# Kernel optimization log

Measured on AMD Instinct MI355X. Metric: run time of the kernel, lower is better.

The kernel has to match this reference:

```python
import jax, jax.numpy as jnp
import numpy as np

SIGMA = 1.0
TEMPERATURE = 1.0
GAMMA = 1.0 / (2.0 * SIGMA ** 2)


def setup_inputs() -> dict:
    key = jax.random.key(0)
    k1, k2 = jax.random.split(key)
    B, N, D = 8, 1024, 128
    features_nc = jax.random.normal(k1, (B, N, D), dtype=jnp.float32)
    features_c = jax.random.normal(k2, (B, N, D), dtype=jnp.float32)
    return {"features_nc": features_nc, "features_c": features_c}


def reference(features_nc, features_c):
    D = features_nc.shape[-1]
    x = features_nc.reshape(-1, D)   # (K, D)
    y = features_c.reshape(-1, D)    # (K, D)
    K = x.shape[0]
    x_sq = jnp.sum(x * x, axis=1, keepdims=True)          # (K, 1)
    y_sq = jnp.sum(y * y, axis=1, keepdims=True)          # (K, 1)
    sq_dist = x_sq + y_sq.T - 2.0 * jnp.matmul(x, y.T)    # (K, K)
    logits = (-GAMMA / TEMPERATURE) * sq_dist
    # cross-entropy with labels = arange(K): mean over rows of -log_softmax diag
    log_probs = jax.nn.log_softmax(logits, axis=-1)
    diag = jnp.diagonal(log_probs)
    loss = -jnp.mean(diag)
    return loss
```

## Files before the change

kernel.cpp:

```cpp
#include <hip/hip_runtime.h>
#include <hip/hip_bf16.h>
#include <math.h>

#define KROWS 8192
#define DDIM  128
#define RT    128
#define CTILE 128
#define NTILES 64
#define NRB   64
#define NC0   12
#define TILEB (CTILE * DDIM * 2)
#define SHIFT 94.0f

static constexpr float LOG2E_F = 1.44269504088896340736f;
static constexpr float LN2_F   = 0.69314718055994530942f;

typedef __attribute__((ext_vector_type(8))) short short8;
typedef __attribute__((ext_vector_type(4))) float float4v;

#if __has_builtin(__builtin_amdgcn_exp2f)
#define EXP2(x) __builtin_amdgcn_exp2f(x)
#else
#define EXP2(x) exp2f(x)
#endif

#define AS1C(p) ((const __attribute__((address_space(1))) void*)(p))
#define AS3(p)  ((__attribute__((address_space(3))) void*)(p))

static __device__ __forceinline__ unsigned short f2bf(float f) {
    __hip_bfloat16 h = __float2bfloat16(f);
    return *reinterpret_cast<unsigned short*>(&h);
}

__global__ __launch_bounds__(256) void prep_kernel(
    const float* __restrict__ x, const float* __restrict__ y,
    unsigned int* __restrict__ xb, unsigned int* __restrict__ yb,
    float* __restrict__ xsq2, float* __restrict__ ysq2,
    float* __restrict__ diagn, float* __restrict__ pl)
{
    const int w = threadIdx.x >> 6, lane = threadIdx.x & 63;
    const int row = blockIdx.x * 4 + w;
    if (blockIdx.x < KROWS / 256) pl[blockIdx.x * 256 + threadIdx.x] = 0.0f;
    const float2 xv = *reinterpret_cast<const float2*>(x + (size_t)row * DDIM + lane * 2);
    const float2 yv = *reinterpret_cast<const float2*>(y + (size_t)row * DDIM + lane * 2);
    xb[(size_t)row * 64 + lane] = (unsigned int)f2bf(xv.x * LOG2E_F)
                                | ((unsigned int)f2bf(xv.y * LOG2E_F) << 16);
    yb[(size_t)row * 64 + lane] = (unsigned int)f2bf(yv.x) | ((unsigned int)f2bf(yv.y) << 16);
    float xx = xv.x * xv.x + xv.y * xv.y;
    float yy = yv.x * yv.x + yv.y * yv.y;
    float xy = xv.x * yv.x + xv.y * yv.y;
    #pragma unroll
    for (int o = 32; o > 0; o >>= 1) {
        xx += __shfl_xor(xx, o, 64);
        yy += __shfl_xor(yy, o, 64);
        xy += __shfl_xor(xy, o, 64);
    }
    if (lane == 0) {
        xsq2[row] = fmaf(-0.5f * xx, LOG2E_F, SHIFT);
        ysq2[row] = -0.5f * yy * LOG2E_F;
        diagn[row] = xy - 0.5f * (xx + yy);
    }
}

__global__ __launch_bounds__(256, 2) void gemm_lse_kernel(
    const unsigned short* __restrict__ xb, const unsigned short* __restrict__ yb,
    const float* __restrict__ xsq2, const float* __restrict__ ysq2,
    float* __restrict__ pl)
{
    __shared__ alignas(16) unsigned char Ys[TILEB];

    const int t = threadIdx.x;
    const int w = t >> 6, lane = t & 63, quad = lane >> 4, lo = lane & 15;
    const int rb = (blockIdx.x & (NRB - 1)) * RT;
    const int c0 = blockIdx.x >> 6;

    short8 af[2][4];
    #pragma unroll
    for (int ri = 0; ri < 2; ri++)
        #pragma unroll
        for (int kk = 0; kk < 4; kk++)
            af[ri][kk] = *reinterpret_cast<const short8*>(
                xb + (size_t)(rb + w * 32 + ri * 16 + lo) * DDIM + kk * 32 + quad * 8);

    float a2v[8];
    #pragma unroll
    for (int ri = 0; ri < 2; ri++)
        #pragma unroll
        for (int r = 0; r < 4; r++)
            a2v[ri * 4 + r] = xsq2[rb + w * 32 + ri * 16 + quad * 4 + r];

    float sums[8];
    #pragma unroll
    for (int i = 0; i < 8; i++) sums[i] = 0.0f;

    const int gswz = ((t >> 4) << 8) + (((t & 15) ^ ((t >> 4) & 7)) << 4);
    int base_k[4];
    #pragma unroll
    for (int kk = 0; kk < 4; kk++)
        base_k[kk] = lo * 256 + ((((kk << 2) + quad) ^ (lo & 7)) << 4);

    {
        const char* g = (const char*)yb + (size_t)c0 * TILEB + gswz;
        #pragma unroll
        for (int q = 0; q < 8; q++)
            __builtin_amdgcn_global_load_lds(AS1C(g + q * 4096),
                                             AS3(&Ys[(q * 256 + t) * 16]), 16, 0, 0);
    }
    __syncthreads();

    int ct = c0;
    while (true) {
        float b2[8];
        #pragma unroll
        for (int ci = 0; ci < 8; ci++) b2[ci] = ysq2[ct * CTILE + ci * 16 + lo];

        float4v acc[2][8];
        #pragma unroll
        for (int ri = 0; ri < 2; ri++)
            #pragma unroll
            for (int ci = 0; ci < 8; ci++)
                acc[ri][ci] = (float4v){a2v[ri * 4 + 0] + b2[ci], a2v[ri * 4 + 1] + b2[ci],
                                        a2v[ri * 4 + 2] + b2[ci], a2v[ri * 4 + 3] + b2[ci]};

        #pragma unroll
        for (int kk = 0; kk < 4; kk++) {
            #pragma unroll
            for (int ci = 0; ci < 8; ci++) {
                short8 b = *reinterpret_cast<const short8*>(&Ys[base_k[kk] + ci * 4096]);
                acc[0][ci] = __builtin_amdgcn_mfma_f32_16x16x32_bf16(af[0][kk], b, acc[0][ci], 0, 0, 0);
                acc[1][ci] = __builtin_amdgcn_mfma_f32_16x16x32_bf16(af[1][kk], b, acc[1][ci], 0, 0, 0);
            }
        }
        __syncthreads();

        const int ctn = ct + NC0;
        if (ctn < NTILES) {
            const char* g = (const char*)yb + (size_t)ctn * TILEB + gswz;
            #pragma unroll
            for (int q = 0; q < 8; q++)
                __builtin_amdgcn_global_load_lds(AS1C(g + q * 4096),
                                                 AS3(&Ys[(q * 256 + t) * 16]), 16, 0, 0);
        }

        #pragma unroll
        for (int ri = 0; ri < 2; ri++)
            #pragma unroll
            for (int r = 0; r < 4; r++) {
                float s = 0.0f;
                #pragma unroll
                for (int ci = 0; ci < 8; ci++)
                    s += EXP2(acc[ri][ci][r]);
                sums[ri * 4 + r] += s;
            }

        if (ctn >= NTILES) break;
        ct = ctn;
        __syncthreads();
    }

    #pragma unroll
    for (int i = 0; i < 8; i++) {
        float s = sums[i];
        s += __shfl_xor(s, 1, 64);
        s += __shfl_xor(s, 2, 64);
        s += __shfl_xor(s, 4, 64);
        s += __shfl_xor(s, 8, 64);
        if (lo == 0) {
            int row = rb + w * 32 + (i >> 2) * 16 + quad * 4 + (i & 3);
            atomicAdd(&pl[row], s);
        }
    }
}

__global__ __launch_bounds__(1024) void finish_kernel(
    const float* __restrict__ pl, const float* __restrict__ diagn,
    float* __restrict__ out)
{
    const int t = threadIdx.x;
    float acc = 0.0f;
    for (int r = t; r < KROWS; r += 1024)
        acc += (log2f(pl[r]) - SHIFT) * LN2_F - diagn[r];
    #pragma unroll
    for (int o = 32; o > 0; o >>= 1) acc += __shfl_down(acc, o, 64);
    __shared__ float ws[16];
    if ((t & 63) == 0) ws[t >> 6] = acc;
    __syncthreads();
    if (t == 0) {
        float s = 0.0f;
        #pragma unroll
        for (int i = 0; i < 16; i++) s += ws[i];
        out[0] = s * (1.0f / KROWS);
    }
}

extern "C" void kernel_launch(void* const* d_in, const int* in_sizes, int n_in,
                              void* d_out, int out_size, void* d_ws, size_t ws_size,
                              hipStream_t stream) {
    const float* x = (const float*)d_in[0];
    const float* y = (const float*)d_in[1];
    float* out = (float*)d_out;

    unsigned short* xb = (unsigned short*)d_ws;
    unsigned short* yb = xb + (size_t)KROWS * DDIM;
    float* xsq2  = (float*)(yb + (size_t)KROWS * DDIM);
    float* ysq2  = xsq2 + KROWS;
    float* diagn = ysq2 + KROWS;
    float* pl    = diagn + KROWS;

    prep_kernel<<<KROWS / 4, 256, 0, stream>>>(x, y, (unsigned int*)xb, (unsigned int*)yb,
                                               xsq2, ysq2, diagn, pl);
    gemm_lse_kernel<<<NRB * NC0, 256, 0, stream>>>(xb, yb, xsq2, ysq2, pl);
    finish_kernel<<<1, 1024, 0, stream>>>(pl, diagn, out);
}
```

Before: 87.56 us.

## Double-buffer Y tiles in LDS and interleave exp with MFMA per column chunk

Replaces the single LDS Y tile with two buffers so the next tile's global-to-LDS load is issued before computing on the current one, dropping one barrier per iteration. It reduces column-split blocks from 12 to 8, so each block processes exactly 8 tiles in a fully unrolled loop. It also restructures the inner loop to finish each 16-column chunk's MFMAs and exponentials before moving on, shrinking the accumulator set and letting exp work overlap matrix ops. The cost is double the LDS footprint, which may limit occupancy, and fewer total blocks (512 vs 768), which may leave CUs underused.

```diff
diff --git a/kernel.cpp b/kernel.cpp
--- a/kernel.cpp
+++ b/kernel.cpp
@@ -8,7 +8,7 @@
 #define CTILE 128
 #define NTILES 64
 #define NRB   64
-#define NC0   12
+#define NC0   8
 #define TILEB (CTILE * DDIM * 2)
 #define SHIFT 94.0f
 
@@ -67,13 +67,24 @@
     const float* __restrict__ xsq2, const float* __restrict__ ysq2,
     float* __restrict__ pl)
 {
-    __shared__ alignas(16) unsigned char Ys[TILEB];
+    __shared__ alignas(16) unsigned char Ys0[TILEB];
+    __shared__ alignas(16) unsigned char Ys1[TILEB];
 
     const int t = threadIdx.x;
     const int w = t >> 6, lane = t & 63, quad = lane >> 4, lo = lane & 15;
     const int rb = (blockIdx.x & (NRB - 1)) * RT;
     const int c0 = blockIdx.x >> 6;
 
+    const int gswz = ((t >> 4) << 8) + (((t & 15) ^ ((t >> 4) & 7)) << 4);
+
+    {
+        const char* g = (const char*)yb + (size_t)c0 * TILEB + gswz;
+        #pragma unroll
+        for (int q = 0; q < 8; q++)
+            __builtin_amdgcn_global_load_lds(AS1C(g + q * 4096),
+                                             AS3(&Ys0[(q * 256 + t) * 16]), 16, 0, 0);
+    }
+
     short8 af[2][4];
     #pragma unroll
     for (int ri = 0; ri < 2; ri++)
@@ -89,73 +100,69 @@
         for (int r = 0; r < 4; r++)
             a2v[ri * 4 + r] = xsq2[rb + w * 32 + ri * 16 + quad * 4 + r];
 
-    float sums[8];
-    #pragma unroll
-    for (int i = 0; i < 8; i++) sums[i] = 0.0f;
-
-    const int gswz = ((t >> 4) << 8) + (((t & 15) ^ ((t >> 4) & 7)) << 4);
+    float b2[8];
+    #pragma unroll
+    for (int ci = 0; ci < 8; ci++) b2[ci] = ysq2[c0 * CTILE + ci * 16 + lo];
+
     int base_k[4];
     #pragma unroll
     for (int kk = 0; kk < 4; kk++)
         base_k[kk] = lo * 256 + ((((kk << 2) + quad) ^ (lo & 7)) << 4);
 
-    {
-        const char* g = (const char*)yb + (size_t)c0 * TILEB + gswz;
-        #pragma unroll
-        for (int q = 0; q < 8; q++)
-            __builtin_amdgcn_global_load_lds(AS1C(g + q * 4096),
-                                             AS3(&Ys[(q * 256 + t) * 16]), 16, 0, 0);
-    }
+    float sums[8];
+    #pragma unroll
+    for (int i = 0; i < 8; i++) sums[i] = 0.0f;
+
     __syncthreads();
 
-    int ct = c0;
-    while (true) {
-        float b2[8];
-        #pragma unroll
-        for (int ci = 0; ci < 8; ci++) b2[ci] = ysq2[ct * CTILE + ci * 16 + lo];
-
-        float4v acc[2][8];
-        #pragma unroll
-        for (int ri = 0; ri < 2; ri++)
-            #pragma unroll
-            for (int ci = 0; ci < 8; ci++)
-                acc[ri][ci] = (float4v){a2v[ri * 4 + 0] + b2[ci], a2v[ri * 4 + 1] + b2[ci],
-                                        a2v[ri * 4 + 2] + b2[ci], a2v[ri * 4 + 3] + b2[ci]};
-
-        #pragma unroll
-        for (int kk = 0; kk < 4; kk++) {
-            #pragma unroll
-            for (int ci = 0; ci < 8; ci++) {
-                short8 b = *reinterpret_cast<const short8*>(&Ys[base_k[kk] + ci * 4096]);
-                acc[0][ci] = __builtin_amdgcn_mfma_f32_16x16x32_bf16(af[0][kk], b, acc[0][ci], 0, 0, 0);
-                acc[1][ci] = __builtin_amdgcn_mfma_f32_16x16x32_bf16(af[1][kk], b, acc[1][ci], 0, 0, 0);
-            }
-        }
-        __syncthreads();
-
-        const int ctn = ct + NC0;
-        if (ctn < NTILES) {
+    #pragma unroll
+    for (int k = 0; k < 8; k++) {
+        const unsigned char* cur = (k & 1) ? Ys1 : Ys0;
+        unsigned char*       nxt = (k & 1) ? Ys0 : Ys1;
+
+        float b2n[8];
+        if (k < 7) {
+            const int ctn = c0 + (k + 1) * NC0;
+            #pragma unroll
+            for (int ci = 0; ci < 8; ci++) b2n[ci] = ysq2[ctn * CTILE + ci * 16 + lo];
             const char* g = (const char*)yb + (size_t)ctn * TILEB + gswz;
             #pragma unroll
             for (int q = 0; q < 8; q++)
                 __builtin_amdgcn_global_load_lds(AS1C(g + q * 4096),
-                                                 AS3(&Ys[(q * 256 + t) * 16]), 16, 0, 0);
-        }
-
-        #pragma unroll
-        for (int ri = 0; ri < 2; ri++)
+                                                 AS3(&nxt[(q * 256 + t) * 16]), 16, 0, 0);
+        }
+
+        float tsum[8];
+        #pragma unroll
+        for (int i = 0; i < 8; i++) tsum[i] = 0.0f;
+
+        #pragma unroll
+        for (int ci = 0; ci < 8; ci++) {
+            float4v a0 = (float4v){a2v[0] + b2[ci], a2v[1] + b2[ci],
+                                   a2v[2] + b2[ci], a2v[3] + b2[ci]};
+            float4v a1 = (float4v){a2v[4] + b2[ci], a2v[5] + b2[ci],
+                                   a2v[6] + b2[ci], a2v[7] + b2[ci]};
+            #pragma unroll
+            for (int kk = 0; kk < 4; kk++) {
+                short8 b = *reinterpret_cast<const short8*>(&cur[base_k[kk] + ci * 4096]);
+                a0 = __builtin_amdgcn_mfma_f32_16x16x32_bf16(af[0][kk], b, a0, 0, 0, 0);
+                a1 = __builtin_amdgcn_mfma_f32_16x16x32_bf16(af[1][kk], b, a1, 0, 0, 0);
+            }
             #pragma unroll
             for (int r = 0; r < 4; r++) {
-                float s = 0.0f;
-                #pragma unroll
-                for (int ci = 0; ci < 8; ci++)
-                    s += EXP2(acc[ri][ci][r]);
-                sums[ri * 4 + r] += s;
+                tsum[r]     += EXP2(a0[r]);
+                tsum[4 + r] += EXP2(a1[r]);
             }
-
-        if (ctn >= NTILES) break;
-        ct = ctn;
-        __syncthreads();
+        }
+
+        #pragma unroll
+        for (int i = 0; i < 8; i++) sums[i] += tsum[i];
+
+        if (k < 7) {
+            #pragma unroll
+            for (int ci = 0; ci < 8; ci++) b2[ci] = b2n[ci];
+            __syncthreads();
+        }
     }
 
     #pragma unroll
```

Result: slower. 167.8 us (+91.6%).

## Restructure tile loop per column group to cut registers and raise occupancy

Applied to the files above, without the earlier changes.

Reorders the inner GEMM loop so each 16-column group runs its full k-reduction and is exponentiated right away, rather than keeping all 16 accumulators live across the tile. This shrinks accumulator register pressure enough to request 4 blocks per CU instead of 2, and NC0 goes from 12 to 16 so more blocks launch. The first Y tile load is also issued before the A-fragment loads so the two overlap. Only the last two column groups are deferred past the barrier to overlap their exp with the next prefetch, which leaves less exp work hidden behind loads and gives each block fewer tiles to amortise setup over.

```diff
diff --git a/kernel.cpp b/kernel.cpp
--- a/kernel.cpp
+++ b/kernel.cpp
@@ -8,7 +8,7 @@
 #define CTILE 128
 #define NTILES 64
 #define NRB   64
-#define NC0   12
+#define NC0   16
 #define TILEB (CTILE * DDIM * 2)
 #define SHIFT 94.0f
 
@@ -62,7 +62,7 @@
     }
 }
 
-__global__ __launch_bounds__(256, 2) void gemm_lse_kernel(
+__global__ __launch_bounds__(256, 4) void gemm_lse_kernel(
     const unsigned short* __restrict__ xb, const unsigned short* __restrict__ yb,
     const float* __restrict__ xsq2, const float* __restrict__ ysq2,
     float* __restrict__ pl)
@@ -74,6 +74,16 @@
     const int rb = (blockIdx.x & (NRB - 1)) * RT;
     const int c0 = blockIdx.x >> 6;
 
+    const int gswz = ((t >> 4) << 8) + (((t & 15) ^ ((t >> 4) & 7)) << 4);
+
+    {
+        const char* g = (const char*)yb + (size_t)c0 * TILEB + gswz;
+        #pragma unroll
+        for (int q = 0; q < 8; q++)
+            __builtin_amdgcn_global_load_lds(AS1C(g + q * 4096),
+                                             AS3(&Ys[(q * 256 + t) * 16]), 16, 0, 0);
+    }
+
     short8 af[2][4];
     #pragma unroll
     for (int ri = 0; ri < 2; ri++)
@@ -89,23 +99,15 @@
         for (int r = 0; r < 4; r++)
             a2v[ri * 4 + r] = xsq2[rb + w * 32 + ri * 16 + quad * 4 + r];
 
-    float sums[8];
-    #pragma unroll
-    for (int i = 0; i < 8; i++) sums[i] = 0.0f;
-
-    const int gswz = ((t >> 4) << 8) + (((t & 15) ^ ((t >> 4) & 7)) << 4);
     int base_k[4];
     #pragma unroll
     for (int kk = 0; kk < 4; kk++)
         base_k[kk] = lo * 256 + ((((kk << 2) + quad) ^ (lo & 7)) << 4);
 
-    {
-        const char* g = (const char*)yb + (size_t)c0 * TILEB + gswz;
-        #pragma unroll
-        for (int q = 0; q < 8; q++)
-            __builtin_amdgcn_global_load_lds(AS1C(g + q * 4096),
-                                             AS3(&Ys[(q * 256 + t) * 16]), 16, 0, 0);
-    }
+    float sums[8];
+    #pragma unroll
+    for (int i = 0; i < 8; i++) sums[i] = 0.0f;
+
     __syncthreads();
 
     int ct = c0;
@@ -114,23 +116,43 @@
         #pragma unroll
         for (int ci = 0; ci < 8; ci++) b2[ci] = ysq2[ct * CTILE + ci * 16 + lo];
 
-        float4v acc[2][8];
-        #pragma unroll
-        for (int ri = 0; ri < 2; ri++)
+        float tsum[8];
+        #pragma unroll
+        for (int i = 0; i < 8; i++) tsum[i] = 0.0f;
+
+        #pragma unroll
+        for (int ci = 0; ci < 6; ci++) {
+            float4v a0 = (float4v){a2v[0] + b2[ci], a2v[1] + b2[ci],
+                                   a2v[2] + b2[ci], a2v[3] + b2[ci]};
+            float4v a1 = (float4v){a2v[4] + b2[ci], a2v[5] + b2[ci],
+                                   a2v[6] + b2[ci], a2v[7] + b2[ci]};
             #pragma unroll
-            for (int ci = 0; ci < 8; ci++)
-                acc[ri][ci] = (float4v){a2v[ri * 4 + 0] + b2[ci], a2v[ri * 4 + 1] + b2[ci],
-                                        a2v[ri * 4 + 2] + b2[ci], a2v[ri * 4 + 3] + b2[ci]};
-
+            for (int kk = 0; kk < 4; kk++) {
+                short8 b = *reinterpret_cast<const short8*>(&Ys[base_k[kk] + ci * 4096]);
+                a0 = __builtin_amdgcn_mfma_f32_16x16x32_bf16(af[0][kk], b, a0, 0, 0, 0);
+                a1 = __builtin_amdgcn_mfma_f32_16x16x32_bf16(af[1][kk], b, a1, 0, 0, 0);
+            }
+            #pragma unroll
+            for (int r = 0; r < 4; r++) {
+                tsum[r]     += EXP2(a0[r]);
+                tsum[4 + r] += EXP2(a1[r]);
+            }
+        }
+
+        float4v a60 = (float4v){a2v[0] + b2[6], a2v[1] + b2[6], a2v[2] + b2[6], a2v[3] + b2[6]};
+        float4v a61 = (float4v){a2v[4] + b2[6], a2v[5] + b2[6], a2v[6] + b2[6], a2v[7] + b2[6]};
+        float4v a70 = (float4v){a2v[0] + b2[7], a2v[1] + b2[7], a2v[2] + b2[7], a2v[3] + b2[7]};
+        float4v a71 = (float4v){a2v[4] + b2[7], a2v[5] + b2[7], a2v[6] + b2[7], a2v[7] + b2[7]};
         #pragma unroll
         for (int kk = 0; kk < 4; kk++) {
-            #pragma unroll
-            for (int ci = 0; ci < 8; ci++) {
-                short8 b = *reinterpret_cast<const short8*>(&Ys[base_k[kk] + ci * 4096]);
-                acc[0][ci] = __builtin_amdgcn_mfma_f32_16x16x32_bf16(af[0][kk], b, acc[0][ci], 0, 0, 0);
-                acc[1][ci] = __builtin_amdgcn_mfma_f32_16x16x32_bf16(af[1][kk], b, acc[1][ci], 0, 0, 0);
-            }
-        }
+            short8 b6 = *reinterpret_cast<const short8*>(&Ys[base_k[kk] + 6 * 4096]);
+            a60 = __builtin_amdgcn_mfma_f32_16x16x32_bf16(af[0][kk], b6, a60, 0, 0, 0);
+            a61 = __builtin_amdgcn_mfma_f32_16x16x32_bf16(af[1][kk], b6, a61, 0, 0, 0);
+            short8 b7 = *reinterpret_cast<const short8*>(&Ys[base_k[kk] + 7 * 4096]);
+            a70 = __builtin_amdgcn_mfma_f32_16x16x32_bf16(af[0][kk], b7, a70, 0, 0, 0);
+            a71 = __builtin_amdgcn_mfma_f32_16x16x32_bf16(af[1][kk], b7, a71, 0, 0, 0);
+        }
+
         __syncthreads();
 
         const int ctn = ct + NC0;
@@ -143,15 +165,17 @@
         }
 
         #pragma unroll
-        for (int ri = 0; ri < 2; ri++)
-            #pragma unroll
-            for (int r = 0; r < 4; r++) {
-                float s = 0.0f;
-                #pragma unroll
-                for (int ci = 0; ci < 8; ci++)
-                    s += EXP2(acc[ri][ci][r]);
-                sums[ri * 4 + r] += s;
-            }
+        for (int r = 0; r < 4; r++) {
+            tsum[r]     += EXP2(a60[r]);
+            tsum[4 + r] += EXP2(a61[r]);
+        }
+        #pragma unroll
+        for (int r = 0; r < 4; r++) {
+            tsum[r]     += EXP2(a70[r]);
+            tsum[4 + r] += EXP2(a71[r]);
+        }
+        #pragma unroll
+        for (int i = 0; i < 8; i++) sums[i] += tsum[i];
 
         if (ctn >= NTILES) break;
         ct = ctn;
```

Result: slower. 90.96 us (+3.9%).
